# Optimization experiments

Hardware: AMD Instinct MI355X
Metric: run time of the kernel (lower is better)

The kernel has to match this reference:

```python
import math
import jax, jax.numpy as jnp
import numpy as np

B, S, D, H = 128, 512, 768, 12
DH = D // H  # 64


def setup_inputs() -> dict:
    key = jax.random.key(0)
    k1, k2, k3, k4, k5 = jax.random.split(key, 5)
    return {
        "X": jax.random.normal(k1, (B, S, D), jnp.float32),
        "W_qkv": jax.random.normal(k2, (3 * D, D), jnp.float32) * 0.02,
        "b_qkv": jax.random.normal(k3, (3 * D,), jnp.float32) * 0.02,
        "W_dense": jax.random.normal(k4, (D, D), jnp.float32) * 0.02,
        "b_dense": jax.random.normal(k5, (D,), jnp.float32) * 0.02,
    }


def reference(X, W_qkv, b_qkv, W_dense, b_dense):
    # Faithful translation of SelfAttention.forward (including its unusual
    # seq/batch layout: scores are [S*H, B, B] and the tril mask FILLS the
    # lower triangle with -10000, exactly as masked_fill_(tril, -1e4) does).
    b, s, d = X.shape
    qkv = jnp.einsum('bsd,ed->bse', X, W_qkv) + b_qkv            # [B,S,3D]
    qkv = qkv.reshape(b, s, H, 3 * DH)
    q = qkv[..., :DH]
    k = qkv[..., DH:2 * DH]
    v = qkv[..., 2 * DH:]
    q = q.reshape(b, s * H, DH).transpose(1, 0, 2)               # [S*H,B,DH]
    k = k.reshape(b, s * H, DH).transpose(1, 0, 2)
    v = v.reshape(b, s * H, DH).transpose(1, 0, 2)
    scores = jnp.einsum('nbd,ncd->nbc', q, k) / math.sqrt(DH)    # [S*H,B,B]
    scores = scores.reshape(s, H, b, b)
    tril = jnp.tril(jnp.ones((s, b, b), bool))[:, None]          # [S,1,B,B]
    scores = jnp.where(tril, jnp.float32(-10000.0), scores)
    probs = jax.nn.softmax(scores, axis=-1).reshape(s * H, b, b)
    ctx = jnp.einsum('nbc,ncd->nbd', probs, v)                   # [S*H,B,DH]
    ctx = ctx.reshape(s, H, b, DH).transpose(2, 0, 1, 3).reshape(b, s, d)
    out = jnp.einsum('bsd,ed->bse', ctx, W_dense)                # bias NOT added
    return (out, b_dense)
```

## Files before the change

kernel.cpp:

```cpp
#include <hip/hip_runtime.h>
#include <hip/hip_bf16.h>
#include <cstdint>
#include <cstddef>


typedef __attribute__((ext_vector_type(8))) short bf16x8_t;
typedef __attribute__((ext_vector_type(4))) float f32x4_t;

__device__ inline unsigned short f2bf(float x) {
  union { float f; unsigned int u; } v; v.f = x;
  return (unsigned short)((v.u + 0x7FFFu + ((v.u >> 16) & 1u)) >> 16);
}

#define GLL16(gp, lp) __builtin_amdgcn_global_load_lds(                      \
    (const __attribute__((address_space(1))) void*)(gp),                     \
    (__attribute__((address_space(3))) void*)(lp), 16, 0, 0)

__global__ __launch_bounds__(256) void cvt_kernel(const float* __restrict__ in,
                                                  unsigned short* __restrict__ out,
                                                  int n4) {
  int i = blockIdx.x * 256 + threadIdx.x;
  if (i >= n4) return;
  const float4 v = ((const float4*)in)[i];
  ushort4 o;
  o.x = f2bf(v.x); o.y = f2bf(v.y); o.z = f2bf(v.z); o.w = f2bf(v.w);
  ((ushort4*)out)[i] = o;
}

__global__ void bias_tail(const float* __restrict__ b, float* __restrict__ out) {
  int i = blockIdx.x * 256 + threadIdx.x;
  if (i < 768) out[(size_t)128 * 512 * 768 + i] = b[i];
}

__global__ __launch_bounds__(256) void gemm_qkv(
    const unsigned short* __restrict__ A,
    const unsigned short* __restrict__ Bt,
    const float* __restrict__ bias,
    unsigned short* __restrict__ QKV) {
  __shared__ unsigned short As[128 * 32];
  __shared__ unsigned short Bs[128 * 32];
  const int tid = threadIdx.x;
  const int wave = tid >> 6, lane = tid & 63;
  const int lane15 = lane & 15, quad = lane >> 4;
  const int mBase = blockIdx.y * 128;
  const int nBase = blockIdx.x * 128;
  const int wm = (wave >> 1) * 64;
  const int wn = (wave & 1) * 64;

  f32x4_t acc[4][4];
#pragma unroll
  for (int i = 0; i < 4; ++i)
#pragma unroll
    for (int j = 0; j < 4; ++j) { f32x4_t z = {0.f, 0.f, 0.f, 0.f}; acc[i][j] = z; }

  const int r16 = lane & 15;
  const int ck8 = (lane >> 4) * 8;
  const unsigned short* Ag = A + (size_t)(mBase + wave * 32 + r16) * 768 + ck8;
  const unsigned short* Bg = Bt + (size_t)(nBase + wave * 32 + r16) * 768 + ck8;
  unsigned short* lA = &As[wave * 1024];
  unsigned short* lB = &Bs[wave * 1024];

  const int aOff = ((wave >> 1) * 4) * 512 + lane * 8;
  const int bOff = ((wave & 1) * 4) * 512 + lane * 8;

  for (int k0 = 0; k0 < 768; k0 += 32) {
    GLL16(Ag + k0, lA);
    GLL16(Ag + 16 * 768 + k0, lA + 512);
    GLL16(Bg + k0, lB);
    GLL16(Bg + 16 * 768 + k0, lB + 512);
    __syncthreads();
    bf16x8_t aF[4], bF[4];
#pragma unroll
    for (int im = 0; im < 4; ++im) aF[im] = *(const bf16x8_t*)&As[aOff + im * 512];
#pragma unroll
    for (int in = 0; in < 4; ++in) bF[in] = *(const bf16x8_t*)&Bs[bOff + in * 512];
#pragma unroll
    for (int im = 0; im < 4; ++im)
#pragma unroll
      for (int in = 0; in < 4; ++in)
        acc[im][in] = __builtin_amdgcn_mfma_f32_16x16x32_bf16(aF[im], bF[in], acc[im][in], 0, 0, 0);
    __syncthreads();
  }

  float bv[4];
#pragma unroll
  for (int in = 0; in < 4; ++in) bv[in] = bias[nBase + wn + in * 16 + lane15];

#pragma unroll
  for (int im = 0; im < 4; ++im) {
#pragma unroll
    for (int r = 0; r < 4; ++r) {
      const int m = mBase + wm + im * 16 + quad * 4 + r;
      unsigned short* orow = QKV + (size_t)m * 2304 + nBase + wn + lane15;
#pragma unroll
      for (int in = 0; in < 4; ++in)
        orow[in * 16] = f2bf(acc[im][in][r] + bv[in]);
    }
  }
}

__global__ __launch_bounds__(256) void attn_kernel(
    const unsigned short* __restrict__ QKV,
    unsigned short* __restrict__ Ctx) {
  __shared__ unsigned short Qs[128 * 72];
  __shared__ unsigned short Ks[128 * 72];
  __shared__ unsigned short Vt[64 * 136];
  __shared__ unsigned short Ps[4][16 * 136];

  const int n = blockIdx.x;
  const int s = n / 12;
  const int h = n - s * 12;
  const int tid = threadIdx.x;
  const int wave = tid >> 6, lane = tid & 63;
  const int lane15 = lane & 15, quad = lane >> 4;

#pragma unroll
  for (int it = 0; it < 4; ++it) {
    const int idx = it * 256 + tid;
    const int bb = idx >> 3, seg = idx & 7;
    const size_t g = (size_t)(bb * 512 + s) * 2304 + h * 192 + seg * 8;
    *(uint4*)&Qs[bb * 72 + seg * 8] = *(const uint4*)&QKV[g];
    *(uint4*)&Ks[bb * 72 + seg * 8] = *(const uint4*)&QKV[g + 64];
  }
  {
    const int c = tid & 127, half = tid >> 7;
    const size_t vb = (size_t)(c * 512 + s) * 2304 + h * 192 + 128;
#pragma unroll
    for (int dd = 0; dd < 4; ++dd) {
      const int dseg = half * 4 + dd;
      uint4 v = *(const uint4*)&QKV[vb + dseg * 8];
      const unsigned short* pv = (const unsigned short*)&v;
#pragma unroll
      for (int j = 0; j < 8; ++j) Vt[(dseg * 8 + j) * 136 + c] = pv[j];
    }
  }
  __syncthreads();

  f32x4_t sc[2][8];
#pragma unroll
  for (int im = 0; im < 2; ++im)
#pragma unroll
    for (int in = 0; in < 8; ++in) { f32x4_t z = {0.f, 0.f, 0.f, 0.f}; sc[im][in] = z; }

#pragma unroll
  for (int kk = 0; kk < 2; ++kk) {
    bf16x8_t a0 = *(const bf16x8_t*)&Qs[(wave * 32 + lane15) * 72 + kk * 32 + quad * 8];
    bf16x8_t a1 = *(const bf16x8_t*)&Qs[(wave * 32 + 16 + lane15) * 72 + kk * 32 + quad * 8];
#pragma unroll
    for (int in = 0; in < 8; ++in) {
      bf16x8_t b = *(const bf16x8_t*)&Ks[(in * 16 + lane15) * 72 + kk * 32 + quad * 8];
      sc[0][in] = __builtin_amdgcn_mfma_f32_16x16x32_bf16(a0, b, sc[0][in], 0, 0, 0);
      sc[1][in] = __builtin_amdgcn_mfma_f32_16x16x32_bf16(a1, b, sc[1][in], 0, 0, 0);
    }
  }

  unsigned short* myP = &Ps[wave][0];

#pragma unroll 1
  for (int im = 0; im < 2; ++im) {
#pragma unroll
    for (int r = 0; r < 4; ++r) {
      const int row = wave * 32 + im * 16 + quad * 4 + r;
      float vals[8];
      float mx = -3.0e38f;
#pragma unroll
      for (int in = 0; in < 8; ++in) {
        const int col = in * 16 + lane15;
        float v = sc[im][in][r] * 0.125f;
        v = (col <= row) ? -10000.0f : v;
        vals[in] = v;
        mx = fmaxf(mx, v);
      }
      mx = fmaxf(mx, __shfl_xor(mx, 1, 16));
      mx = fmaxf(mx, __shfl_xor(mx, 2, 16));
      mx = fmaxf(mx, __shfl_xor(mx, 4, 16));
      mx = fmaxf(mx, __shfl_xor(mx, 8, 16));
      float sum = 0.f;
#pragma unroll
      for (int in = 0; in < 8; ++in) {
        const float e_ = __expf(vals[in] - mx);
        vals[in] = e_;
        sum += e_;
      }
      sum += __shfl_xor(sum, 1, 16);
      sum += __shfl_xor(sum, 2, 16);
      sum += __shfl_xor(sum, 4, 16);
      sum += __shfl_xor(sum, 8, 16);
      const float inv = 1.0f / sum;
#pragma unroll
      for (int in = 0; in < 8; ++in)
        myP[(quad * 4 + r) * 136 + in * 16 + lane15] = f2bf(vals[in] * inv);
    }
    __syncthreads();

    f32x4_t oc[4];
#pragma unroll
    for (int nt = 0; nt < 4; ++nt) { f32x4_t z = {0.f, 0.f, 0.f, 0.f}; oc[nt] = z; }
#pragma unroll
    for (int kk = 0; kk < 4; ++kk) {
      bf16x8_t a = *(const bf16x8_t*)&myP[lane15 * 136 + kk * 32 + quad * 8];
#pragma unroll
      for (int nt = 0; nt < 4; ++nt) {
        bf16x8_t b = *(const bf16x8_t*)&Vt[(nt * 16 + lane15) * 136 + kk * 32 + quad * 8];
        oc[nt] = __builtin_amdgcn_mfma_f32_16x16x32_bf16(a, b, oc[nt], 0, 0, 0);
      }
    }
#pragma unroll
    for (int nt = 0; nt < 4; ++nt) {
#pragma unroll
      for (int r = 0; r < 4; ++r) {
        const int bb = wave * 32 + im * 16 + quad * 4 + r;
        Ctx[((size_t)bb * 512 + s) * 768 + h * 64 + nt * 16 + lane15] = f2bf(oc[nt][r]);
      }
    }
    __syncthreads();
  }
}

__global__ __launch_bounds__(256) void gemm_out(
    const unsigned short* __restrict__ A,
    const unsigned short* __restrict__ Bt,
    float* __restrict__ Out) {
  __shared__ unsigned short As[128 * 32];
  __shared__ unsigned short Bs[128 * 32];
  const int tid = threadIdx.x;
  const int wave = tid >> 6, lane = tid & 63;
  const int lane15 = lane & 15, quad = lane >> 4;
  const int mBase = blockIdx.y * 128;
  const int nBase = blockIdx.x * 128;
  const int wm = (wave >> 1) * 64;
  const int wn = (wave & 1) * 64;

  f32x4_t acc[4][4];
#pragma unroll
  for (int i = 0; i < 4; ++i)
#pragma unroll
    for (int j = 0; j < 4; ++j) { f32x4_t z = {0.f, 0.f, 0.f, 0.f}; acc[i][j] = z; }

  const int r16 = lane & 15;
  const int ck8 = (lane >> 4) * 8;
  const unsigned short* Ag = A + (size_t)(mBase + wave * 32 + r16) * 768 + ck8;
  const unsigned short* Bg = Bt + (size_t)(nBase + wave * 32 + r16) * 768 + ck8;
  unsigned short* lA = &As[wave * 1024];
  unsigned short* lB = &Bs[wave * 1024];

  const int aOff = ((wave >> 1) * 4) * 512 + lane * 8;
  const int bOff = ((wave & 1) * 4) * 512 + lane * 8;

  for (int k0 = 0; k0 < 768; k0 += 32) {
    GLL16(Ag + k0, lA);
    GLL16(Ag + 16 * 768 + k0, lA + 512);
    GLL16(Bg + k0, lB);
    GLL16(Bg + 16 * 768 + k0, lB + 512);
    __syncthreads();
    bf16x8_t aF[4], bF[4];
#pragma unroll
    for (int im = 0; im < 4; ++im) aF[im] = *(const bf16x8_t*)&As[aOff + im * 512];
#pragma unroll
    for (int in = 0; in < 4; ++in) bF[in] = *(const bf16x8_t*)&Bs[bOff + in * 512];
#pragma unroll
    for (int im = 0; im < 4; ++im)
#pragma unroll
      for (int in = 0; in < 4; ++in)
        acc[im][in] = __builtin_amdgcn_mfma_f32_16x16x32_bf16(aF[im], bF[in], acc[im][in], 0, 0, 0);
    __syncthreads();
  }

#pragma unroll
  for (int im = 0; im < 4; ++im) {
#pragma unroll
    for (int r = 0; r < 4; ++r) {
      const int m = mBase + wm + im * 16 + quad * 4 + r;
      float* orow = Out + (size_t)m * 768 + nBase + wn + lane15;
#pragma unroll
      for (int in = 0; in < 4; ++in)
        orow[in * 16] = acc[im][in][r];
    }
  }
}

extern "C" void kernel_launch(void* const* d_in, const int* in_sizes, int n_in,
                              void* d_out, int out_size, void* d_ws, size_t ws_size,
                              hipStream_t stream) {
  const float* X    = (const float*)d_in[0];
  const float* Wqkv = (const float*)d_in[1];
  const float* bqkv = (const float*)d_in[2];
  const float* Wd   = (const float*)d_in[3];
  const float* bd   = (const float*)d_in[4];
  float* out = (float*)d_out;

  char* ws = (char*)d_ws;
  unsigned short* Xb  = (unsigned short*)(ws);
  unsigned short* QKV = (unsigned short*)(ws + 100663296);
  unsigned short* Wqb = (unsigned short*)(ws + 402653184);
  unsigned short* Wdb = (unsigned short*)(ws + 406192128);

  cvt_kernel<<<dim3(49152), 256, 0, stream>>>(X, Xb, 12582912);
  cvt_kernel<<<dim3(1728), 256, 0, stream>>>(Wqkv, Wqb, 442368);
  cvt_kernel<<<dim3(576), 256, 0, stream>>>(Wd, Wdb, 147456);
  bias_tail<<<dim3(3), 256, 0, stream>>>(bd, out);

  gemm_qkv<<<dim3(18, 512), 256, 0, stream>>>(Xb, Wqb, bqkv, QKV);
  attn_kernel<<<dim3(6144), 256, 0, stream>>>(QKV, Xb );
  gemm_out<<<dim3(6, 512), 256, 0, stream>>>(Xb, Wdb, out);
}
```

Baseline: 1.260 ms.

## Double GEMM K-step, swap grid order, and alias attention LDS buffers

Both GEMMs now stage a 64-wide K slice per barrier pair instead of 32, which halves the number of __syncthreads per tile and gives each wave more MFMAs between barriers. The grid is transposed so consecutive blocks walk M while sharing the same weight N tile, which should improve L2 reuse of the weights. The attention kernel computes QK^T first and then reuses the Q/K shared buffers for V-transpose and P, cutting LDS use per block to raise occupancy. The cost is an extra barrier and serializing the V load after the score MMA, so that load can no longer overlap with it.

```diff
diff --git a/kernel.cpp b/kernel.cpp
--- a/kernel.cpp
+++ b/kernel.cpp
@@ -37,13 +37,13 @@
     const unsigned short* __restrict__ Bt,
     const float* __restrict__ bias,
     unsigned short* __restrict__ QKV) {
-  __shared__ unsigned short As[128 * 32];
-  __shared__ unsigned short Bs[128 * 32];
+  __shared__ unsigned short As[128 * 64];
+  __shared__ unsigned short Bs[128 * 64];
   const int tid = threadIdx.x;
   const int wave = tid >> 6, lane = tid & 63;
   const int lane15 = lane & 15, quad = lane >> 4;
-  const int mBase = blockIdx.y * 128;
-  const int nBase = blockIdx.x * 128;
+  const int mBase = blockIdx.x * 128;
+  const int nBase = blockIdx.y * 128;
   const int wm = (wave >> 1) * 64;
   const int wn = (wave & 1) * 64;
 
@@ -57,28 +57,37 @@
   const int ck8 = (lane >> 4) * 8;
   const unsigned short* Ag = A + (size_t)(mBase + wave * 32 + r16) * 768 + ck8;
   const unsigned short* Bg = Bt + (size_t)(nBase + wave * 32 + r16) * 768 + ck8;
-  unsigned short* lA = &As[wave * 1024];
-  unsigned short* lB = &Bs[wave * 1024];
-
-  const int aOff = ((wave >> 1) * 4) * 512 + lane * 8;
-  const int bOff = ((wave & 1) * 4) * 512 + lane * 8;
-
-  for (int k0 = 0; k0 < 768; k0 += 32) {
+  unsigned short* lA = &As[wave * 4 * 512];
+  unsigned short* lB = &Bs[wave * 4 * 512];
+
+  const int aSub = (wm >> 4) * 2;
+  const int bSub = (wn >> 4) * 2;
+
+  for (int k0 = 0; k0 < 768; k0 += 64) {
     GLL16(Ag + k0, lA);
-    GLL16(Ag + 16 * 768 + k0, lA + 512);
+    GLL16(Ag + k0 + 32, lA + 512);
+    GLL16(Ag + 16 * 768 + k0, lA + 1024);
+    GLL16(Ag + 16 * 768 + k0 + 32, lA + 1536);
     GLL16(Bg + k0, lB);
-    GLL16(Bg + 16 * 768 + k0, lB + 512);
-    __syncthreads();
-    bf16x8_t aF[4], bF[4];
-#pragma unroll
-    for (int im = 0; im < 4; ++im) aF[im] = *(const bf16x8_t*)&As[aOff + im * 512];
-#pragma unroll
-    for (int in = 0; in < 4; ++in) bF[in] = *(const bf16x8_t*)&Bs[bOff + in * 512];
-#pragma unroll
-    for (int im = 0; im < 4; ++im)
+    GLL16(Bg + k0 + 32, lB + 512);
+    GLL16(Bg + 16 * 768 + k0, lB + 1024);
+    GLL16(Bg + 16 * 768 + k0 + 32, lB + 1536);
+    __syncthreads();
+#pragma unroll
+    for (int kh = 0; kh < 2; ++kh) {
+      bf16x8_t aF[4], bF[4];
+#pragma unroll
+      for (int im = 0; im < 4; ++im)
+        aF[im] = *(const bf16x8_t*)&As[(aSub + im * 2 + kh) * 512 + lane * 8];
 #pragma unroll
       for (int in = 0; in < 4; ++in)
-        acc[im][in] = __builtin_amdgcn_mfma_f32_16x16x32_bf16(aF[im], bF[in], acc[im][in], 0, 0, 0);
+        bF[in] = *(const bf16x8_t*)&Bs[(bSub + in * 2 + kh) * 512 + lane * 8];
+#pragma unroll
+      for (int im = 0; im < 4; ++im)
+#pragma unroll
+        for (int in = 0; in < 4; ++in)
+          acc[im][in] = __builtin_amdgcn_mfma_f32_16x16x32_bf16(aF[im], bF[in], acc[im][in], 0, 0, 0);
+    }
     __syncthreads();
   }
 
@@ -104,8 +113,6 @@
     unsigned short* __restrict__ Ctx) {
   __shared__ unsigned short Qs[128 * 72];
   __shared__ unsigned short Ks[128 * 72];
-  __shared__ unsigned short Vt[64 * 136];
-  __shared__ unsigned short Ps[4][16 * 136];
 
   const int n = blockIdx.x;
   const int s = n / 12;
@@ -122,6 +129,29 @@
     *(uint4*)&Qs[bb * 72 + seg * 8] = *(const uint4*)&QKV[g];
     *(uint4*)&Ks[bb * 72 + seg * 8] = *(const uint4*)&QKV[g + 64];
   }
+  __syncthreads();
+
+  f32x4_t sc[2][8];
+#pragma unroll
+  for (int im = 0; im < 2; ++im)
+#pragma unroll
+    for (int in = 0; in < 8; ++in) { f32x4_t z = {0.f, 0.f, 0.f, 0.f}; sc[im][in] = z; }
+
+#pragma unroll
+  for (int kk = 0; kk < 2; ++kk) {
+    bf16x8_t a0 = *(const bf16x8_t*)&Qs[(wave * 32 + lane15) * 72 + kk * 32 + quad * 8];
+    bf16x8_t a1 = *(const bf16x8_t*)&Qs[(wave * 32 + 16 + lane15) * 72 + kk * 32 + quad * 8];
+#pragma unroll
+    for (int in = 0; in < 8; ++in) {
+      bf16x8_t b = *(const bf16x8_t*)&Ks[(in * 16 + lane15) * 72 + kk * 32 + quad * 8];
+      sc[0][in] = __builtin_amdgcn_mfma_f32_16x16x32_bf16(a0, b, sc[0][in], 0, 0, 0);
+      sc[1][in] = __builtin_amdgcn_mfma_f32_16x16x32_bf16(a1, b, sc[1][in], 0, 0, 0);
+    }
+  }
+  __syncthreads();
+
+  unsigned short* Vt = Ks;
+  unsigned short* Ps = Qs;
   {
     const int c = tid & 127, half = tid >> 7;
     const size_t vb = (size_t)(c * 512 + s) * 2304 + h * 192 + 128;
@@ -134,27 +164,8 @@
       for (int j = 0; j < 8; ++j) Vt[(dseg * 8 + j) * 136 + c] = pv[j];
     }
   }
-  __syncthreads();
-
-  f32x4_t sc[2][8];
-#pragma unroll
-  for (int im = 0; im < 2; ++im)
-#pragma unroll
-    for (int in = 0; in < 8; ++in) { f32x4_t z = {0.f, 0.f, 0.f, 0.f}; sc[im][in] = z; }
-
-#pragma unroll
-  for (int kk = 0; kk < 2; ++kk) {
-    bf16x8_t a0 = *(const bf16x8_t*)&Qs[(wave * 32 + lane15) * 72 + kk * 32 + quad * 8];
-    bf16x8_t a1 = *(const bf16x8_t*)&Qs[(wave * 32 + 16 + lane15) * 72 + kk * 32 + quad * 8];
-#pragma unroll
-    for (int in = 0; in < 8; ++in) {
-      bf16x8_t b = *(const bf16x8_t*)&Ks[(in * 16 + lane15) * 72 + kk * 32 + quad * 8];
-      sc[0][in] = __builtin_amdgcn_mfma_f32_16x16x32_bf16(a0, b, sc[0][in], 0, 0, 0);
-      sc[1][in] = __builtin_amdgcn_mfma_f32_16x16x32_bf16(a1, b, sc[1][in], 0, 0, 0);
-    }
-  }
-
-  unsigned short* myP = &Ps[wave][0];
+
+  unsigned short* myP = Ps + wave * 16 * 136;
 
 #pragma unroll 1
   for (int im = 0; im < 2; ++im) {
@@ -221,13 +232,13 @@
     const unsigned short* __restrict__ A,
     const unsigned short* __restrict__ Bt,
     float* __restrict__ Out) {
-  __shared__ unsigned short As[128 * 32];
-  __shared__ unsigned short Bs[128 * 32];
+  __shared__ unsigned short As[128 * 64];
+  __shared__ unsigned short Bs[128 * 64];
   const int tid = threadIdx.x;
   const int wave = tid >> 6, lane = tid & 63;
   const int lane15 = lane & 15, quad = lane >> 4;
-  const int mBase = blockIdx.y * 128;
-  const int nBase = blockIdx.x * 128;
+  const int mBase = blockIdx.x * 128;
+  const int nBase = blockIdx.y * 128;
   const int wm = (wave >> 1) * 64;
   const int wn = (wave & 1) * 64;
 
@@ -241,28 +252,37 @@
   const int ck8 = (lane >> 4) * 8;
   const unsigned short* Ag = A + (size_t)(mBase + wave * 32 + r16) * 768 + ck8;
   const unsigned short* Bg = Bt + (size_t)(nBase + wave * 32 + r16) * 768 + ck8;
-  unsigned short* lA = &As[wave * 1024];
-  unsigned short* lB = &Bs[wave * 1024];
-
-  const int aOff = ((wave >> 1) * 4) * 512 + lane * 8;
-  const int bOff = ((wave & 1) * 4) * 512 + lane * 8;
-
-  for (int k0 = 0; k0 < 768; k0 += 32) {
+  unsigned short* lA = &As[wave * 4 * 512];
+  unsigned short* lB = &Bs[wave * 4 * 512];
+
+  const int aSub = (wm >> 4) * 2;
+  const int bSub = (wn >> 4) * 2;
+
+  for (int k0 = 0; k0 < 768; k0 += 64) {
     GLL16(Ag + k0, lA);
-    GLL16(Ag + 16 * 768 + k0, lA + 512);
+    GLL16(Ag + k0 + 32, lA + 512);
+    GLL16(Ag + 16 * 768 + k0, lA + 1024);
+    GLL16(Ag + 16 * 768 + k0 + 32, lA + 1536);
     GLL16(Bg + k0, lB);
-    GLL16(Bg + 16 * 768 + k0, lB + 512);
-    __syncthreads();
-    bf16x8_t aF[4], bF[4];
-#pragma unroll
-    for (int im = 0; im < 4; ++im) aF[im] = *(const bf16x8_t*)&As[aOff + im * 512];
-#pragma unroll
-    for (int in = 0; in < 4; ++in) bF[in] = *(const bf16x8_t*)&Bs[bOff + in * 512];
-#pragma unroll
-    for (int im = 0; im < 4; ++im)
+    GLL16(Bg + k0 + 32, lB + 512);
+    GLL16(Bg + 16 * 768 + k0, lB + 1024);
+    GLL16(Bg + 16 * 768 + k0 + 32, lB + 1536);
+    __syncthreads();
+#pragma unroll
+    for (int kh = 0; kh < 2; ++kh) {
+      bf16x8_t aF[4], bF[4];
+#pragma unroll
+      for (int im = 0; im < 4; ++im)
+        aF[im] = *(const bf16x8_t*)&As[(aSub + im * 2 + kh) * 512 + lane * 8];
 #pragma unroll
       for (int in = 0; in < 4; ++in)
-        acc[im][in] = __builtin_amdgcn_mfma_f32_16x16x32_bf16(aF[im], bF[in], acc[im][in], 0, 0, 0);
+        bF[in] = *(const bf16x8_t*)&Bs[(bSub + in * 2 + kh) * 512 + lane * 8];
+#pragma unroll
+      for (int im = 0; im < 4; ++im)
+#pragma unroll
+        for (int in = 0; in < 4; ++in)
+          acc[im][in] = __builtin_amdgcn_mfma_f32_16x16x32_bf16(aF[im], bF[in], acc[im][in], 0, 0, 0);
+    }
     __syncthreads();
   }
 
@@ -300,7 +320,7 @@
   cvt_kernel<<<dim3(576), 256, 0, stream>>>(Wd, Wdb, 147456);
   bias_tail<<<dim3(3), 256, 0, stream>>>(bd, out);
 
-  gemm_qkv<<<dim3(18, 512), 256, 0, stream>>>(Xb, Wqb, bqkv, QKV);
+  gemm_qkv<<<dim3(512, 18), 256, 0, stream>>>(Xb, Wqb, bqkv, QKV);
   attn_kernel<<<dim3(6144), 256, 0, stream>>>(QKV, Xb );
-  gemm_out<<<dim3(6, 512), 256, 0, stream>>>(Xb, Wdb, out);
-}
+  gemm_out<<<dim3(512, 6), 256, 0, stream>>>(Xb, Wdb, out);
+}
```

Result: no change. 1.257 ms (-0.2%).
